# Kernel optimization log

Hardware: AMD Instinct MI355X
Metric: run time of the kernel (lower is better)

The kernel has to match this reference:

```python
import jax, jax.numpy as jnp
import numpy as np

N, E, D, ED = 50000, 800000, 64, 2


def setup_inputs() -> dict:
    key = jax.random.key(0)
    ks = jax.random.split(key, 16)
    inp = {
        "h": jax.random.normal(ks[0], (N, D), jnp.float32),
        "coord": jax.random.normal(ks[1], (N, 3), jnp.float32),
        "edge_index": jax.random.randint(ks[2], (2, E), 0, N, jnp.int32),
        "edge_attr": jax.random.normal(ks[3], (E, ED), jnp.float32),
        # edge_mlp: Linear(2D+1+ED -> D), Linear(D -> D)
        "W_e1": jax.random.normal(ks[4], (2 * D + 1 + ED, D), jnp.float32) * 0.08,
        "b_e1": jnp.zeros((D,), jnp.float32),
        "W_e2": jax.random.normal(ks[5], (D, D), jnp.float32) * 0.12,
        "b_e2": jnp.zeros((D,), jnp.float32),
        # node_mlp: Linear(D+D -> D), Linear(D -> D)
        "W_n1": jax.random.normal(ks[6], (2 * D, D), jnp.float32) * 0.08,
        "b_n1": jnp.zeros((D,), jnp.float32),
        "W_n2": jax.random.normal(ks[7], (D, D), jnp.float32) * 0.12,
        "b_n2": jnp.zeros((D,), jnp.float32),
        # coord_mlp: Linear(D -> D), Linear(D -> 1, bias=False, xavier gain 0.001)
        "W_c1": jax.random.normal(ks[8], (D, D), jnp.float32) * 0.12,
        "b_c1": jnp.zeros((D,), jnp.float32),
        "W_c2": jax.random.normal(ks[9], (D, 1), jnp.float32) * 1e-3,
    }
    return inp


def reference(h, coord, edge_index, edge_attr,
              W_e1, b_e1, W_e2, b_e2,
              W_n1, b_n1, W_n2, b_n2,
              W_c1, b_c1, W_c2):
    row, col = edge_index[0], edge_index[1]
    n_nodes = h.shape[0]

    # coord2radial
    coord_diff = coord[row] - coord[col]                       # [E,3]
    radial = jnp.sum(coord_diff * coord_diff, axis=-1, keepdims=True)  # [E,1]

    # edge_model
    e_in = jnp.concatenate([h[row], h[col], radial, edge_attr], axis=-1)  # [E, 2D+1+ED]
    e = jax.nn.silu(e_in @ W_e1 + b_e1)
    edge_feat = jax.nn.silu(e @ W_e2 + b_e2)                   # [E,D]

    # coord_model: trans = coord_diff * coord_mlp(edge_feat), clamp, segment mean
    scale = jax.nn.silu(edge_feat @ W_c1 + b_c1) @ W_c2        # [E,1]
    trans = jnp.clip(coord_diff * scale, -100.0, 100.0)        # [E,3]
    agg_c = jax.ops.segment_sum(trans, row, num_segments=n_nodes)       # [N,3]
    cnt = jax.ops.segment_sum(jnp.ones((trans.shape[0],), trans.dtype), row,
                              num_segments=n_nodes)            # [N]
    coord_out = coord + agg_c / jnp.clip(cnt, 1.0, None)[:, None]  # coords_weight=1.0

    # node_model: segment sum of edge_feat by row, node MLP, residual
    agg_h = jax.ops.segment_sum(edge_feat, row, num_segments=n_nodes)   # [N,D]
    n_in = jnp.concatenate([h, agg_h], axis=-1)                # [N,2D]
    h_out = h + (jax.nn.silu(n_in @ W_n1 + b_n1) @ W_n2 + b_n2)

    return (h_out, coord_out)
```

## Files before the change

### kernel.cpp

```cpp
#include <hip/hip_runtime.h>

#define DD 64
#define NTE 512
#define SLOTMAX 64

using s8v   = __attribute__((ext_vector_type(8))) short;
using f32x4 = __attribute__((ext_vector_type(4))) float;

typedef unsigned int   uint_t;
typedef unsigned short ushort_t;

__device__ __forceinline__ float silu_f(float x) {
    return x / (1.0f + __expf(-x));
}
__device__ __forceinline__ float clamp100(float x) {
    return fminf(fmaxf(x, -100.0f), 100.0f);
}
__device__ __forceinline__ unsigned short f2bf(float x) {
    unsigned int u = __float_as_uint(x);
    return (unsigned short)((u + 0x7FFFu + ((u >> 16) & 1u)) >> 16);
}

#define WAVE_FENCE() do { asm volatile("s_waitcnt lgkmcnt(0)" ::: "memory"); \
                          __builtin_amdgcn_sched_barrier(0); } while (0)

__global__ __launch_bounds__(256) void prep_all(
    const float* __restrict__ h,
    const float* __restrict__ We1, const float* __restrict__ We2,
    const float* __restrict__ Wc1,
    const float* __restrict__ Wn1, const float* __restrict__ Wn2,
    const int*   __restrict__ ei,
    ushort_t* __restrict__ hbf,
    ushort_t* __restrict__ wf,
    int* __restrict__ cnt_i,
    int* __restrict__ slots,
    int E, int total8, int histBlocks, int hbfBlocks)
{
    const int b = blockIdx.x;
    if (b < histBlocks) {
        const int e = b * 256 + threadIdx.x;
        if (e < E) {
            const int r = ei[e];
            const int s = atomicAdd(&cnt_i[r], 1);
            if (s < SLOTMAX) slots[(size_t)r * SLOTMAX + s] = e;
        }
    } else if (b < histBlocks + hbfBlocks) {
        const int t = (b - histBlocks) * 256 + threadIdx.x;
        if (t < total8) {
            const float4 v0 = ((const float4*)h)[t * 2 + 0];
            const float4 v1 = ((const float4*)h)[t * 2 + 1];
            uint4 o;
            o.x = (uint_t)f2bf(v0.x) | ((uint_t)f2bf(v0.y) << 16);
            o.y = (uint_t)f2bf(v0.z) | ((uint_t)f2bf(v0.w) << 16);
            o.z = (uint_t)f2bf(v1.x) | ((uint_t)f2bf(v1.y) << 16);
            o.w = (uint_t)f2bf(v1.z) | ((uint_t)f2bf(v1.w) << 16);
            ((uint4*)hbf)[t] = o;
        }
    } else {
        const int t = (b - histBlocks - hbfBlocks) * 256 + threadIdx.x;
        if (t < 7 * 4096) {
            const int j    = t & 7;
            const int lane = (t >> 3) & 63;
            const int n0   = (t >> 9) & 3;
            const int k0   = (t >> 11) & 1;
            const int mat  = t >> 12;
            const int k = k0 * 32 + ((lane >> 4) * 8) + j;
            const int n = n0 * 16 + (lane & 15);
            float v;
            if      (mat == 0) v = We1[(size_t)k * 64 + n];
            else if (mat == 1) v = We1[(size_t)(64 + k) * 64 + n];
            else if (mat == 2) v = We2[(size_t)k * 64 + n];
            else if (mat == 3) v = Wc1[(size_t)k * 64 + n];
            else if (mat == 4) v = Wn1[(size_t)k * 64 + n];
            else if (mat == 5) v = Wn1[(size_t)(64 + k) * 64 + n];
            else               v = Wn2[(size_t)k * 64 + n];
            wf[t] = f2bf(v);
        }
    }
}

__global__ __launch_bounds__(NTE, 4) void egcl_edge(
    const ushort_t* __restrict__ hbf,
    const ushort_t* __restrict__ wfG,
    const float* __restrict__ coord,
    const int*   __restrict__ ei,
    const float* __restrict__ ea,
    const float* __restrict__ We1,
    const float* __restrict__ be1,
    const float* __restrict__ be2,
    const float* __restrict__ bc1,
    const float* __restrict__ Wc2,
    const int* __restrict__ cnt_i,
    const int* __restrict__ slots,
    ushort_t* __restrict__ aggbf,
    float* __restrict__ coord_out,
    int N, int E, int totalWaves)
{
    __shared__ ushort_t fragLDS[16384];
    __shared__ ushort_t ldsY[8][16 * 72];

    const int tid = threadIdx.x;
    #pragma unroll
    for (int i = 0; i < 4; ++i)
        ((uint4*)fragLDS)[tid + i * 512] = ((const uint4*)wfG)[tid + i * 512];
    __syncthreads();

    const int wid  = tid >> 6;
    const int lane = tid & 63;
    const int l15  = lane & 15;
    const int g    = lane >> 4;

#define LD_WF(mat, k0, n0) \
    (*(const s8v*)(fragLDS + ((((mat)*2 + (k0))*4 + (n0)) * 512) + lane * 8))

    float be1_c[4], w128_c[4], w129_c[4], w130_c[4], be2_c[4], bc1_c[4], wc2_c[4];
    #pragma unroll
    for (int n0 = 0; n0 < 4; ++n0) {
        const int n = n0 * 16 + l15;
        be1_c[n0]  = be1[n];
        w128_c[n0] = We1[128 * 64 + n];
        w129_c[n0] = We1[129 * 64 + n];
        w130_c[n0] = We1[130 * 64 + n];
        be2_c[n0]  = be2[n];
        bc1_c[n0]  = bc1[n];
        wc2_c[n0]  = Wc2[n];
    }

    ushort_t* yw = ldsY[wid];
    const ushort_t* yrow = yw + l15 * 72;

    for (int n = blockIdx.x * 8 + wid; n < N; n += totalWaves) {
        const int deg = cnt_i[n];
        const int effdeg = deg < SLOTMAX ? deg : SLOTMAX;
        const float cnx = coord[n * 3 + 0];
        const float cny = coord[n * 3 + 1];
        const float cnz = coord[n * 3 + 2];

        const ushort_t* hn = hbf + (size_t)n * 64;
        const s8v aN0 = *(const s8v*)(hn + g * 8);
        const s8v aN1 = *(const s8v*)(hn + 32 + g * 8);
        f32x4 rowacc[4];
        #pragma unroll
        for (int n0 = 0; n0 < 4; ++n0) {
            f32x4 a = {0.f, 0.f, 0.f, 0.f};
            a = __builtin_amdgcn_mfma_f32_16x16x32_bf16(aN0, LD_WF(0, 0, n0), a, 0, 0, 0);
            a = __builtin_amdgcn_mfma_f32_16x16x32_bf16(aN1, LD_WF(0, 1, n0), a, 0, 0, 0);
            rowacc[n0] = a;
        }

        float hsum[4] = {0.f, 0.f, 0.f, 0.f};
        float txs = 0.f, tys = 0.f, tzs = 0.f;
        const int ntile = (effdeg + 15) >> 4;

        for (int t = 0; t < ntile; ++t) {
            const int s = t * 16 + l15;
            const bool val = (s < effdeg);
            const int eL = slots[(size_t)n * SLOTMAX + (val ? s : 0)];
            const int ci = ei[E + eL];
            const float cx = coord[ci * 3 + 0];
            const float cy = coord[ci * 3 + 1];
            const float cz = coord[ci * 3 + 2];
            const float dx = cnx - cx, dy = cny - cy, dz = cnz - cz;
            const float radial = dx * dx + dy * dy + dz * dz;
            const float2 a2 = *(const float2*)(ea + (size_t)eL * 2);
            const ushort_t* hc = hbf + (size_t)ci * 64;
            const s8v aC0 = *(const s8v*)(hc + g * 8);
            const s8v aC1 = *(const s8v*)(hc + 32 + g * 8);

            f32x4 acc[4];
            #pragma unroll
            for (int n0 = 0; n0 < 4; ++n0) {
                f32x4 a = rowacc[n0];
                a = __builtin_amdgcn_mfma_f32_16x16x32_bf16(aC0, LD_WF(1, 0, n0), a, 0, 0, 0);
                a = __builtin_amdgcn_mfma_f32_16x16x32_bf16(aC1, LD_WF(1, 1, n0), a, 0, 0, 0);
                acc[n0] = a;
            }

            #pragma unroll
            for (int jj = 0; jj < 4; ++jj) {
                const int m = g * 4 + jj;
                const float rad_m = __shfl(radial, m, 16);
                const float a0_m  = __shfl(a2.x,  m, 16);
                const float a1_m  = __shfl(a2.y,  m, 16);
                #pragma unroll
                for (int n0 = 0; n0 < 4; ++n0) {
                    float y = acc[n0][jj] + be1_c[n0] + rad_m * w128_c[n0]
                            + a0_m * w129_c[n0] + a1_m * w130_c[n0];
                    yw[m * 72 + n0 * 16 + l15] = f2bf(silu_f(y));
                }
            }
            WAVE_FENCE();

            {
                const s8v b0 = *(const s8v*)(yrow + g * 8);
                const s8v b1 = *(const s8v*)(yrow + 32 + g * 8);
                #pragma unroll
                for (int n0 = 0; n0 < 4; ++n0) {
                    f32x4 a = {0.f, 0.f, 0.f, 0.f};
                    a = __builtin_amdgcn_mfma_f32_16x16x32_bf16(b0, LD_WF(2, 0, n0), a, 0, 0, 0);
                    a = __builtin_amdgcn_mfma_f32_16x16x32_bf16(b1, LD_WF(2, 1, n0), a, 0, 0, 0);
                    #pragma unroll
                    for (int jj = 0; jj < 4; ++jj) {
                        const float y2 = silu_f(a[jj] + be2_c[n0]);
                        const bool vj = (t * 16 + g * 4 + jj) < effdeg;
                        hsum[n0] += vj ? y2 : 0.0f;
                        yw[(g * 4 + jj) * 72 + n0 * 16 + l15] = f2bf(y2);
                    }
                }
            }
            WAVE_FENCE();

            {
                const s8v c0 = *(const s8v*)(yrow + g * 8);
                const s8v c1 = *(const s8v*)(yrow + 32 + g * 8);
                float p[4] = {0.f, 0.f, 0.f, 0.f};
                #pragma unroll
                for (int n0 = 0; n0 < 4; ++n0) {
                    f32x4 a = {0.f, 0.f, 0.f, 0.f};
                    a = __builtin_amdgcn_mfma_f32_16x16x32_bf16(c0, LD_WF(3, 0, n0), a, 0, 0, 0);
                    a = __builtin_amdgcn_mfma_f32_16x16x32_bf16(c1, LD_WF(3, 1, n0), a, 0, 0, 0);
                    #pragma unroll
                    for (int jj = 0; jj < 4; ++jj)
                        p[jj] += silu_f(a[jj] + bc1_c[n0]) * wc2_c[n0];
                }
                #pragma unroll
                for (int jj = 0; jj < 4; ++jj) {
                    p[jj] += __shfl_xor(p[jj], 1, 64);
                    p[jj] += __shfl_xor(p[jj], 2, 64);
                    p[jj] += __shfl_xor(p[jj], 4, 64);
                    p[jj] += __shfl_xor(p[jj], 8, 64);
                }
                #pragma unroll
                for (int jj = 0; jj < 4; ++jj) {
                    const int m = g * 4 + jj;
                    if (l15 == m && (t * 16 + m) < effdeg) {
                        const float sc = p[jj];
                        txs += clamp100(dx * sc);
                        tys += clamp100(dy * sc);
                        tzs += clamp100(dz * sc);
                    }
                }
            }
        }

        #pragma unroll
        for (int n0 = 0; n0 < 4; ++n0) {
            hsum[n0] += __shfl_xor(hsum[n0], 16, 64);
            hsum[n0] += __shfl_xor(hsum[n0], 32, 64);
        }
        if (g == 0) {
            #pragma unroll
            for (int n0 = 0; n0 < 4; ++n0)
                aggbf[(size_t)n * 64 + n0 * 16 + l15] = f2bf(hsum[n0]);
        }
        #pragma unroll
        for (int msk = 1; msk < 64; msk <<= 1) {
            txs += __shfl_xor(txs, msk, 64);
            tys += __shfl_xor(tys, msk, 64);
            tzs += __shfl_xor(tzs, msk, 64);
        }
        if (lane == 0) {
            const float inv = 1.0f / fmaxf((float)deg, 1.0f);
            coord_out[(size_t)n * 3 + 0] = cnx + txs * inv;
            coord_out[(size_t)n * 3 + 1] = cny + tys * inv;
            coord_out[(size_t)n * 3 + 2] = cnz + tzs * inv;
        }
    }
#undef LD_WF
}

__global__ __launch_bounds__(NTE, 4) void egcl_node(
    const ushort_t* __restrict__ hbf,
    const ushort_t* __restrict__ aggbf,
    const ushort_t* __restrict__ wfG,
    const float* __restrict__ h,
    const float* __restrict__ bn1,
    const float* __restrict__ bn2,
    float* __restrict__ h_out,
    int N)
{
    __shared__ ushort_t fragLDS[12288];
    __shared__ ushort_t ldsY[8][16 * 72];

    const int tid = threadIdx.x;
    #pragma unroll
    for (int i = 0; i < 3; ++i)
        ((uint4*)fragLDS)[tid + i * 512] = ((const uint4*)(wfG + 16384))[tid + i * 512];
    __syncthreads();

    const int wid  = tid >> 6;
    const int lane = tid & 63;
    const int l15  = lane & 15;
    const int g    = lane >> 4;

#define LD_WN(mat, k0, n0) \
    (*(const s8v*)(fragLDS + ((((mat)*2 + (k0))*4 + (n0)) * 512) + lane * 8))

    float bn1_c[4], bn2_c[4];
    #pragma unroll
    for (int n0 = 0; n0 < 4; ++n0) {
        bn1_c[n0] = bn1[n0 * 16 + l15];
        bn2_c[n0] = bn2[n0 * 16 + l15];
    }

    const int wg = blockIdx.x * 8 + wid;
    const int nb = wg * 16;
    if (nb >= N) return;

    const int nod  = nb + l15;
    const int nodL = nod < N ? nod : N - 1;
    const ushort_t* hrow = hbf   + (size_t)nodL * 64;
    const ushort_t* arow = aggbf + (size_t)nodL * 64;
    const s8v aH0 = *(const s8v*)(hrow + g * 8);
    const s8v aH1 = *(const s8v*)(hrow + 32 + g * 8);
    const s8v aG0 = *(const s8v*)(arow + g * 8);
    const s8v aG1 = *(const s8v*)(arow + 32 + g * 8);

    ushort_t* yw = ldsY[wid];
    #pragma unroll
    for (int n0 = 0; n0 < 4; ++n0) {
        f32x4 a = {0.f, 0.f, 0.f, 0.f};
        a = __builtin_amdgcn_mfma_f32_16x16x32_bf16(aH0, LD_WN(0, 0, n0), a, 0, 0, 0);
        a = __builtin_amdgcn_mfma_f32_16x16x32_bf16(aH1, LD_WN(0, 1, n0), a, 0, 0, 0);
        a = __builtin_amdgcn_mfma_f32_16x16x32_bf16(aG0, LD_WN(1, 0, n0), a, 0, 0, 0);
        a = __builtin_amdgcn_mfma_f32_16x16x32_bf16(aG1, LD_WN(1, 1, n0), a, 0, 0, 0);
        #pragma unroll
        for (int jj = 0; jj < 4; ++jj)
            yw[(g * 4 + jj) * 72 + n0 * 16 + l15] = f2bf(silu_f(a[jj] + bn1_c[n0]));
    }
    WAVE_FENCE();

    const ushort_t* yrow = yw + l15 * 72;
    const s8v b0 = *(const s8v*)(yrow + g * 8);
    const s8v b1 = *(const s8v*)(yrow + 32 + g * 8);
    #pragma unroll
    for (int n0 = 0; n0 < 4; ++n0) {
        f32x4 a = {0.f, 0.f, 0.f, 0.f};
        a = __builtin_amdgcn_mfma_f32_16x16x32_bf16(b0, LD_WN(2, 0, n0), a, 0, 0, 0);
        a = __builtin_amdgcn_mfma_f32_16x16x32_bf16(b1, LD_WN(2, 1, n0), a, 0, 0, 0);
        #pragma unroll
        for (int jj = 0; jj < 4; ++jj) {
            const int m = nb + g * 4 + jj;
            if (m < N) {
                const size_t idx = (size_t)m * 64 + n0 * 16 + l15;
                h_out[idx] = h[idx] + (a[jj] + bn2_c[n0]);
            }
        }
    }
#undef LD_WN
}

extern "C" void kernel_launch(void* const* d_in, const int* in_sizes, int n_in,
                              void* d_out, int out_size, void* d_ws, size_t ws_size,
                              hipStream_t stream) {
    const float* h     = (const float*)d_in[0];
    const float* coord = (const float*)d_in[1];
    const int*   ei    = (const int*)  d_in[2];
    const float* ea    = (const float*)d_in[3];
    const float* We1   = (const float*)d_in[4];
    const float* be1   = (const float*)d_in[5];
    const float* We2   = (const float*)d_in[6];
    const float* be2   = (const float*)d_in[7];
    const float* Wn1   = (const float*)d_in[8];
    const float* bn1   = (const float*)d_in[9];
    const float* Wn2   = (const float*)d_in[10];
    const float* bn2   = (const float*)d_in[11];
    const float* Wc1   = (const float*)d_in[12];
    const float* bc1   = (const float*)d_in[13];
    const float* Wc2   = (const float*)d_in[14];

    const int N = in_sizes[0] / DD;
    const int E = in_sizes[3] / 2;

    float* out       = (float*)d_out;
    float* h_out     = out;
    float* coord_out = out + (size_t)N * DD;

    char* base = (char*)d_ws;
    ushort_t* hbf   = (ushort_t*)base;
    const size_t o_wf    = (size_t)N * DD * 2;
    ushort_t* wf    = (ushort_t*)(base + o_wf);
    const size_t o_agg   = o_wf + 7 * 4096 * 2;
    ushort_t* aggbf = (ushort_t*)(base + o_agg);
    const size_t o_cnt   = o_agg + (size_t)N * DD * 2;
    int* cnt_i      = (int*)(base + o_cnt);
    const size_t o_slots = o_cnt + (size_t)N * 4;
    int* slots      = (int*)(base + o_slots);

    hipMemsetAsync((void*)cnt_i, 0, (size_t)N * 4, stream);

    const int histBlocks = (E + 255) / 256;
    const int total8     = N * DD / 8;
    const int hbfBlocks  = (total8 + 255) / 256;
    const int wfBlocks   = (7 * 4096 + 255) / 256;
    prep_all<<<histBlocks + hbfBlocks + wfBlocks, 256, 0, stream>>>(
        h, We1, We2, Wc1, Wn1, Wn2, ei, hbf, wf, cnt_i, slots,
        E, total8, histBlocks, hbfBlocks);

    const int eblocks = 768;
    const int totalWaves = eblocks * 8;
    egcl_edge<<<eblocks, NTE, 0, stream>>>(
        hbf, wf, coord, ei, ea, We1, be1, be2, bc1, Wc2,
        cnt_i, slots, aggbf, coord_out, N, E, totalWaves);

    const int nwaves  = (N + 15) / 16;
    const int nblocks = (nwaves + 7) / 8;
    egcl_node<<<nblocks, NTE, 0, stream>>>(
        hbf, aggbf, wf, h, bn1, bn2, h_out, N);
}
```

Measured before the change: 255.3 us.

## Transpose edge MLP MFMAs to keep activations in registers, fold biases into MFMA

Swaps MFMA operand roles so edge features live as the B operand: each layer's output fragment is converted with packed bf16 conversion and fed straight into the next layer. This removes the per-wave LDS staging buffer and its wave fences. Radial, edge attributes and all biases are folded into extra MFMA K-slices using a constant-1 lane, with the matching weight fragments precomputed in prep. It also prefetches the next node's degree and slot list, and lowers the edge block count. The cost is extra MFMAs and bf16 rounding of the biases and radial, plus a reduction pattern whose correctness depends on the new fragment layout (note the 0.25 factor on the inverse count).

```diff
diff --git a/kernel.cpp b/kernel.cpp
--- a/kernel.cpp
+++ b/kernel.cpp
@@ -10,6 +10,8 @@
 typedef unsigned int   uint_t;
 typedef unsigned short ushort_t;
 
+union U8 { s8v v; uint_t u[4]; };
+
 __device__ __forceinline__ float silu_f(float x) {
     return x / (1.0f + __expf(-x));
 }
@@ -19,6 +21,11 @@
 __device__ __forceinline__ unsigned short f2bf(float x) {
     unsigned int u = __float_as_uint(x);
     return (unsigned short)((u + 0x7FFFu + ((u >> 16) & 1u)) >> 16);
+}
+__device__ __forceinline__ uint_t cvt_pk_bf16(float lo, float hi) {
+    uint_t r;
+    asm("v_cvt_pk_bf16_f32 %0, %1, %2" : "=v"(r) : "v"(lo), "v"(hi));
+    return r;
 }
 
 #define WAVE_FENCE() do { asm volatile("s_waitcnt lgkmcnt(0)" ::: "memory"); \
@@ -29,6 +36,8 @@
     const float* __restrict__ We1, const float* __restrict__ We2,
     const float* __restrict__ Wc1,
     const float* __restrict__ Wn1, const float* __restrict__ Wn2,
+    const float* __restrict__ be1, const float* __restrict__ be2,
+    const float* __restrict__ bc1,
     const int*   __restrict__ ei,
     ushort_t* __restrict__ hbf,
     ushort_t* __restrict__ wf,
@@ -58,13 +67,17 @@
         }
     } else {
         const int t = (b - histBlocks - hbfBlocks) * 256 + threadIdx.x;
-        if (t < 7 * 4096) {
+        if (t >= 32768) return;
+        if (t < 28672) {
             const int j    = t & 7;
             const int lane = (t >> 3) & 63;
             const int n0   = (t >> 9) & 3;
             const int k0   = (t >> 11) & 1;
             const int mat  = t >> 12;
-            const int k = k0 * 32 + ((lane >> 4) * 8) + j;
+            const int g    = lane >> 4;
+            int k;
+            if (mat == 2 || mat == 3) k = 16 * (2 * k0 + (j >> 2)) + 4 * g + (j & 3);
+            else                      k = k0 * 32 + g * 8 + j;
             const int n = n0 * 16 + (lane & 15);
             float v;
             if      (mat == 0) v = We1[(size_t)k * 64 + n];
@@ -75,6 +88,25 @@
             else if (mat == 5) v = Wn1[(size_t)(64 + k) * 64 + n];
             else               v = Wn2[(size_t)k * 64 + n];
             wf[t] = f2bf(v);
+        } else {
+            const int t2   = t - 28672;
+            const int j    = t2 & 7;
+            const int lane = (t2 >> 3) & 63;
+            const int n0   = (t2 >> 9) & 3;
+            const int xm   = (t2 >> 11) & 1;
+            const int k = 8 * (lane >> 4) + j;
+            const int m = n0 * 16 + (lane & 15);
+            float v = 0.0f;
+            if (xm == 0) {
+                if      (k == 0) v = We1[(size_t)128 * 64 + m];
+                else if (k == 1) v = We1[(size_t)129 * 64 + m];
+                else if (k == 2) v = We1[(size_t)130 * 64 + m];
+                else if (k == 3) v = be1[m];
+            } else {
+                if      (k == 0) v = be2[m];
+                else if (k == 1) v = bc1[m];
+            }
+            wf[t] = f2bf(v);
         }
     }
 }
@@ -85,10 +117,6 @@
     const float* __restrict__ coord,
     const int*   __restrict__ ei,
     const float* __restrict__ ea,
-    const float* __restrict__ We1,
-    const float* __restrict__ be1,
-    const float* __restrict__ be2,
-    const float* __restrict__ bc1,
     const float* __restrict__ Wc2,
     const int* __restrict__ cnt_i,
     const int* __restrict__ slots,
@@ -96,13 +124,13 @@
     float* __restrict__ coord_out,
     int N, int E, int totalWaves)
 {
-    __shared__ ushort_t fragLDS[16384];
-    __shared__ ushort_t ldsY[8][16 * 72];
+    __shared__ ushort_t fragLDS[20480];
 
     const int tid = threadIdx.x;
     #pragma unroll
     for (int i = 0; i < 4; ++i)
         ((uint4*)fragLDS)[tid + i * 512] = ((const uint4*)wfG)[tid + i * 512];
+    ((uint4*)fragLDS)[2048 + tid] = ((const uint4*)wfG)[3584 + tid];
     __syncthreads();
 
     const int wid  = tid >> 6;
@@ -110,52 +138,73 @@
     const int l15  = lane & 15;
     const int g    = lane >> 4;
 
-#define LD_WF(mat, k0, n0) \
-    (*(const s8v*)(fragLDS + ((((mat)*2 + (k0))*4 + (n0)) * 512) + lane * 8))
-
-    float be1_c[4], w128_c[4], w129_c[4], w130_c[4], be2_c[4], bc1_c[4], wc2_c[4];
-    #pragma unroll
-    for (int n0 = 0; n0 < 4; ++n0) {
-        const int n = n0 * 16 + l15;
-        be1_c[n0]  = be1[n];
-        w128_c[n0] = We1[128 * 64 + n];
-        w129_c[n0] = We1[129 * 64 + n];
-        w130_c[n0] = We1[130 * 64 + n];
-        be2_c[n0]  = be2[n];
-        bc1_c[n0]  = bc1[n];
-        wc2_c[n0]  = Wc2[n];
-    }
-
-    ushort_t* yw = ldsY[wid];
-    const ushort_t* yrow = yw + l15 * 72;
-
-    for (int n = blockIdx.x * 8 + wid; n < N; n += totalWaves) {
-        const int deg = cnt_i[n];
+#define LD_W(mat, k0, m0) \
+    (*(const s8v*)(fragLDS + ((((mat)*2 + (k0))*4 + (m0)) * 512) + lane * 8))
+#define LD_X7(m0) (*(const s8v*)(fragLDS + 16384 + (m0) * 512 + lane * 8))
+#define LD_XB(m0) (*(const s8v*)(fragLDS + 18432 + (m0) * 512 + lane * 8))
+
+    float wc2_c[4][4];
+    #pragma unroll
+    for (int m0 = 0; m0 < 4; ++m0)
+        #pragma unroll
+        for (int j = 0; j < 4; ++j)
+            wc2_c[m0][j] = Wc2[m0 * 16 + 4 * g + j];
+
+    U8 b2f, bcf;
+    b2f.u[0] = 0x00003F80u; b2f.u[1] = 0; b2f.u[2] = 0; b2f.u[3] = 0;
+    bcf.u[0] = 0x3F800000u; bcf.u[1] = 0; bcf.u[2] = 0; bcf.u[3] = 0;
+
+    const f32x4 zero4 = {0.f, 0.f, 0.f, 0.f};
+
+    int n = blockIdx.x * 8 + wid;
+    int pdeg = 0, pslot = 0;
+    if (n < N) {
+        pdeg  = cnt_i[n];
+        pslot = slots[(size_t)n * SLOTMAX + l15];
+    }
+
+    for (; n < N; n += totalWaves) {
+        const int deg   = pdeg;
+        const int slot0 = pslot;
+        const int nn = n + totalWaves;
+        if (nn < N) {
+            pdeg  = cnt_i[nn];
+            pslot = slots[(size_t)nn * SLOTMAX + l15];
+        }
+
         const int effdeg = deg < SLOTMAX ? deg : SLOTMAX;
         const float cnx = coord[n * 3 + 0];
         const float cny = coord[n * 3 + 1];
         const float cnz = coord[n * 3 + 2];
+        const int slot0_l0 = __shfl(slot0, lane & 48, 64);
 
         const ushort_t* hn = hbf + (size_t)n * 64;
-        const s8v aN0 = *(const s8v*)(hn + g * 8);
-        const s8v aN1 = *(const s8v*)(hn + 32 + g * 8);
+        const s8v bn0 = *(const s8v*)(hn + g * 8);
+        const s8v bn1 = *(const s8v*)(hn + 32 + g * 8);
         f32x4 rowacc[4];
         #pragma unroll
-        for (int n0 = 0; n0 < 4; ++n0) {
-            f32x4 a = {0.f, 0.f, 0.f, 0.f};
-            a = __builtin_amdgcn_mfma_f32_16x16x32_bf16(aN0, LD_WF(0, 0, n0), a, 0, 0, 0);
-            a = __builtin_amdgcn_mfma_f32_16x16x32_bf16(aN1, LD_WF(0, 1, n0), a, 0, 0, 0);
-            rowacc[n0] = a;
-        }
-
-        float hsum[4] = {0.f, 0.f, 0.f, 0.f};
+        for (int m0 = 0; m0 < 4; ++m0) {
+            f32x4 a = zero4;
+            a = __builtin_amdgcn_mfma_f32_16x16x32_bf16(LD_W(0, 0, m0), bn0, a, 0, 0, 0);
+            a = __builtin_amdgcn_mfma_f32_16x16x32_bf16(LD_W(0, 1, m0), bn1, a, 0, 0, 0);
+            rowacc[m0] = a;
+        }
+
+        float hsum[4][4];
+        #pragma unroll
+        for (int m0 = 0; m0 < 4; ++m0)
+            #pragma unroll
+            for (int j = 0; j < 4; ++j) hsum[m0][j] = 0.f;
         float txs = 0.f, tys = 0.f, tzs = 0.f;
+
         const int ntile = (effdeg + 15) >> 4;
-
         for (int t = 0; t < ntile; ++t) {
             const int s = t * 16 + l15;
             const bool val = (s < effdeg);
-            const int eL = slots[(size_t)n * SLOTMAX + (val ? s : 0)];
+            int eL;
+            if (t == 0) eL = val ? slot0 : slot0_l0;
+            else        eL = slots[(size_t)n * SLOTMAX + (val ? s : 0)];
+
             const int ci = ei[E + eL];
             const float cx = coord[ci * 3 + 0];
             const float cy = coord[ci * 3 + 1];
@@ -164,94 +213,100 @@
             const float radial = dx * dx + dy * dy + dz * dz;
             const float2 a2 = *(const float2*)(ea + (size_t)eL * 2);
             const ushort_t* hc = hbf + (size_t)ci * 64;
-            const s8v aC0 = *(const s8v*)(hc + g * 8);
-            const s8v aC1 = *(const s8v*)(hc + 32 + g * 8);
-
-            f32x4 acc[4];
-            #pragma unroll
-            for (int n0 = 0; n0 < 4; ++n0) {
-                f32x4 a = rowacc[n0];
-                a = __builtin_amdgcn_mfma_f32_16x16x32_bf16(aC0, LD_WF(1, 0, n0), a, 0, 0, 0);
-                a = __builtin_amdgcn_mfma_f32_16x16x32_bf16(aC1, LD_WF(1, 1, n0), a, 0, 0, 0);
-                acc[n0] = a;
-            }
-
-            #pragma unroll
-            for (int jj = 0; jj < 4; ++jj) {
-                const int m = g * 4 + jj;
-                const float rad_m = __shfl(radial, m, 16);
-                const float a0_m  = __shfl(a2.x,  m, 16);
-                const float a1_m  = __shfl(a2.y,  m, 16);
+            const s8v bc0 = *(const s8v*)(hc + g * 8);
+            const s8v bc1v = *(const s8v*)(hc + 32 + g * 8);
+
+            U8 ex;
+            ex.u[0] = cvt_pk_bf16(radial, a2.x);
+            ex.u[1] = cvt_pk_bf16(a2.y, 1.0f);
+            ex.u[2] = 0; ex.u[3] = 0;
+
+            f32x4 c1[4];
+            #pragma unroll
+            for (int m0 = 0; m0 < 4; ++m0) {
+                f32x4 a = rowacc[m0];
+                a = __builtin_amdgcn_mfma_f32_16x16x32_bf16(LD_W(1, 0, m0), bc0,  a, 0, 0, 0);
+                a = __builtin_amdgcn_mfma_f32_16x16x32_bf16(LD_W(1, 1, m0), bc1v, a, 0, 0, 0);
+                a = __builtin_amdgcn_mfma_f32_16x16x32_bf16(LD_X7(m0),      ex.v, a, 0, 0, 0);
+                c1[m0] = a;
+            }
+
+            U8 f2a, f2b;
+            #pragma unroll
+            for (int m0 = 0; m0 < 4; ++m0) {
+                const float ya = silu_f(c1[m0][0]);
+                const float yb = silu_f(c1[m0][1]);
+                const float yc = silu_f(c1[m0][2]);
+                const float yd = silu_f(c1[m0][3]);
+                U8& dst = (m0 < 2) ? f2a : f2b;
+                dst.u[(m0 & 1) * 2 + 0] = cvt_pk_bf16(ya, yb);
+                dst.u[(m0 & 1) * 2 + 1] = cvt_pk_bf16(yc, yd);
+            }
+
+            f32x4 c2[4];
+            #pragma unroll
+            for (int m0 = 0; m0 < 4; ++m0) {
+                f32x4 a = zero4;
+                a = __builtin_amdgcn_mfma_f32_16x16x32_bf16(LD_W(2, 0, m0), f2a.v, a, 0, 0, 0);
+                a = __builtin_amdgcn_mfma_f32_16x16x32_bf16(LD_W(2, 1, m0), f2b.v, a, 0, 0, 0);
+                a = __builtin_amdgcn_mfma_f32_16x16x32_bf16(LD_XB(m0),      b2f.v, a, 0, 0, 0);
+                c2[m0] = a;
+            }
+
+            U8 f3a, f3b;
+            #pragma unroll
+            for (int m0 = 0; m0 < 4; ++m0) {
+                const float ya = silu_f(c2[m0][0]);
+                const float yb = silu_f(c2[m0][1]);
+                const float yc = silu_f(c2[m0][2]);
+                const float yd = silu_f(c2[m0][3]);
+                hsum[m0][0] += val ? ya : 0.f;
+                hsum[m0][1] += val ? yb : 0.f;
+                hsum[m0][2] += val ? yc : 0.f;
+                hsum[m0][3] += val ? yd : 0.f;
+                U8& dst = (m0 < 2) ? f3a : f3b;
+                dst.u[(m0 & 1) * 2 + 0] = cvt_pk_bf16(ya, yb);
+                dst.u[(m0 & 1) * 2 + 1] = cvt_pk_bf16(yc, yd);
+            }
+
+            float p = 0.f;
+            #pragma unroll
+            for (int m0 = 0; m0 < 4; ++m0) {
+                f32x4 a = zero4;
+                a = __builtin_amdgcn_mfma_f32_16x16x32_bf16(LD_W(3, 0, m0), f3a.v, a, 0, 0, 0);
+                a = __builtin_amdgcn_mfma_f32_16x16x32_bf16(LD_W(3, 1, m0), f3b.v, a, 0, 0, 0);
+                a = __builtin_amdgcn_mfma_f32_16x16x32_bf16(LD_XB(m0),      bcf.v, a, 0, 0, 0);
                 #pragma unroll
-                for (int n0 = 0; n0 < 4; ++n0) {
-                    float y = acc[n0][jj] + be1_c[n0] + rad_m * w128_c[n0]
-                            + a0_m * w129_c[n0] + a1_m * w130_c[n0];
-                    yw[m * 72 + n0 * 16 + l15] = f2bf(silu_f(y));
-                }
-            }
-            WAVE_FENCE();
-
-            {
-                const s8v b0 = *(const s8v*)(yrow + g * 8);
-                const s8v b1 = *(const s8v*)(yrow + 32 + g * 8);
-                #pragma unroll
-                for (int n0 = 0; n0 < 4; ++n0) {
-                    f32x4 a = {0.f, 0.f, 0.f, 0.f};
-                    a = __builtin_amdgcn_mfma_f32_16x16x32_bf16(b0, LD_WF(2, 0, n0), a, 0, 0, 0);
-                    a = __builtin_amdgcn_mfma_f32_16x16x32_bf16(b1, LD_WF(2, 1, n0), a, 0, 0, 0);
-                    #pragma unroll
-                    for (int jj = 0; jj < 4; ++jj) {
-                        const float y2 = silu_f(a[jj] + be2_c[n0]);
-                        const bool vj = (t * 16 + g * 4 + jj) < effdeg;
-                        hsum[n0] += vj ? y2 : 0.0f;
-                        yw[(g * 4 + jj) * 72 + n0 * 16 + l15] = f2bf(y2);
-                    }
-                }
-            }
-            WAVE_FENCE();
-
-            {
-                const s8v c0 = *(const s8v*)(yrow + g * 8);
-                const s8v c1 = *(const s8v*)(yrow + 32 + g * 8);
-                float p[4] = {0.f, 0.f, 0.f, 0.f};
-                #pragma unroll
-                for (int n0 = 0; n0 < 4; ++n0) {
-                    f32x4 a = {0.f, 0.f, 0.f, 0.f};
-                    a = __builtin_amdgcn_mfma_f32_16x16x32_bf16(c0, LD_WF(3, 0, n0), a, 0, 0, 0);
-                    a = __builtin_amdgcn_mfma_f32_16x16x32_bf16(c1, LD_WF(3, 1, n0), a, 0, 0, 0);
-                    #pragma unroll
-                    for (int jj = 0; jj < 4; ++jj)
-                        p[jj] += silu_f(a[jj] + bc1_c[n0]) * wc2_c[n0];
-                }
-                #pragma unroll
-                for (int jj = 0; jj < 4; ++jj) {
-                    p[jj] += __shfl_xor(p[jj], 1, 64);
-                    p[jj] += __shfl_xor(p[jj], 2, 64);
-                    p[jj] += __shfl_xor(p[jj], 4, 64);
-                    p[jj] += __shfl_xor(p[jj], 8, 64);
-                }
-                #pragma unroll
-                for (int jj = 0; jj < 4; ++jj) {
-                    const int m = g * 4 + jj;
-                    if (l15 == m && (t * 16 + m) < effdeg) {
-                        const float sc = p[jj];
-                        txs += clamp100(dx * sc);
-                        tys += clamp100(dy * sc);
-                        tzs += clamp100(dz * sc);
-                    }
-                }
-            }
-        }
-
-        #pragma unroll
-        for (int n0 = 0; n0 < 4; ++n0) {
-            hsum[n0] += __shfl_xor(hsum[n0], 16, 64);
-            hsum[n0] += __shfl_xor(hsum[n0], 32, 64);
-        }
-        if (g == 0) {
-            #pragma unroll
-            for (int n0 = 0; n0 < 4; ++n0)
-                aggbf[(size_t)n * 64 + n0 * 16 + l15] = f2bf(hsum[n0]);
+                for (int j = 0; j < 4; ++j)
+                    p = fmaf(silu_f(a[j]), wc2_c[m0][j], p);
+            }
+            p += __shfl_xor(p, 16, 64);
+            p += __shfl_xor(p, 32, 64);
+            const float sc = val ? p : 0.f;
+            txs += clamp100(dx * sc);
+            tys += clamp100(dy * sc);
+            tzs += clamp100(dz * sc);
+        }
+
+        #pragma unroll
+        for (int m0 = 0; m0 < 4; ++m0) {
+            #pragma unroll
+            for (int j = 0; j < 4; ++j) {
+                float v = hsum[m0][j];
+                v += __shfl_xor(v, 1, 64);
+                v += __shfl_xor(v, 2, 64);
+                v += __shfl_xor(v, 4, 64);
+                v += __shfl_xor(v, 8, 64);
+                hsum[m0][j] = v;
+            }
+        }
+        if (l15 == 0) {
+            uint_t* ab = (uint_t*)aggbf + (size_t)n * 32 + 2 * g;
+            #pragma unroll
+            for (int m0 = 0; m0 < 4; ++m0) {
+                ab[8 * m0 + 0] = cvt_pk_bf16(hsum[m0][0], hsum[m0][1]);
+                ab[8 * m0 + 1] = cvt_pk_bf16(hsum[m0][2], hsum[m0][3]);
+            }
         }
         #pragma unroll
         for (int msk = 1; msk < 64; msk <<= 1) {
@@ -260,13 +315,15 @@
             tzs += __shfl_xor(tzs, msk, 64);
         }
         if (lane == 0) {
-            const float inv = 1.0f / fmaxf((float)deg, 1.0f);
+            const float inv = 0.25f / fmaxf((float)deg, 1.0f);
             coord_out[(size_t)n * 3 + 0] = cnx + txs * inv;
             coord_out[(size_t)n * 3 + 1] = cny + tys * inv;
             coord_out[(size_t)n * 3 + 2] = cnz + tzs * inv;
         }
     }
-#undef LD_WF
+#undef LD_W
+#undef LD_X7
+#undef LD_XB
 }
 
 __global__ __launch_bounds__(NTE, 4) void egcl_node(
@@ -380,7 +437,7 @@
     ushort_t* hbf   = (ushort_t*)base;
     const size_t o_wf    = (size_t)N * DD * 2;
     ushort_t* wf    = (ushort_t*)(base + o_wf);
-    const size_t o_agg   = o_wf + 7 * 4096 * 2;
+    const size_t o_agg   = o_wf + 32768 * 2;
     ushort_t* aggbf = (ushort_t*)(base + o_agg);
     const size_t o_cnt   = o_agg + (size_t)N * DD * 2;
     int* cnt_i      = (int*)(base + o_cnt);
@@ -392,15 +449,15 @@
     const int histBlocks = (E + 255) / 256;
     const int total8     = N * DD / 8;
     const int hbfBlocks  = (total8 + 255) / 256;
-    const int wfBlocks   = (7 * 4096 + 255) / 256;
+    const int wfBlocks   = (32768 + 255) / 256;
     prep_all<<<histBlocks + hbfBlocks + wfBlocks, 256, 0, stream>>>(
-        h, We1, We2, Wc1, Wn1, Wn2, ei, hbf, wf, cnt_i, slots,
-        E, total8, histBlocks, hbfBlocks);
-
-    const int eblocks = 768;
+        h, We1, We2, Wc1, Wn1, Wn2, be1, be2, bc1, ei,
+        hbf, wf, cnt_i, slots, E, total8, histBlocks, hbfBlocks);
+
+    const int eblocks = 512;
     const int totalWaves = eblocks * 8;
     egcl_edge<<<eblocks, NTE, 0, stream>>>(
-        hbf, wf, coord, ei, ea, We1, be1, be2, bc1, Wc2,
+        hbf, wf, coord, ei, ea, Wc2,
         cnt_i, slots, aggbf, coord_out, N, E, totalWaves);
 
     const int nwaves  = (N + 15) / 16;
```

New measurement: 250.4 us. No clear change (-1.9%).
